# Kernel optimization log

Measured on AMD Instinct MI355X. Metric: run time of the kernel, lower is better.

Reference implementation:

```python
import jax, jax.numpy as jnp
import numpy as np

N = 50000
D = 128
E = 600000
R = 8


def setup_inputs() -> dict:
    key = jax.random.key(0)
    ks = jax.random.split(key, 8)
    x = jax.random.normal(ks[0], (N, D), dtype=jnp.float32)
    edge_index = jax.random.randint(ks[1], (2, E), 0, N, dtype=jnp.int64)
    edge_type = jax.random.randint(ks[2], (E,), 0, R, dtype=jnp.int64)
    scale = 1.0 / np.sqrt(D)
    w1 = jax.random.normal(ks[3], (R, D, D), dtype=jnp.float32) * scale
    root1 = jax.random.normal(ks[4], (D, D), dtype=jnp.float32) * scale
    b1 = jnp.zeros((D,), dtype=jnp.float32)
    w2 = jax.random.normal(ks[5], (R, D, D), dtype=jnp.float32) * scale
    root2 = jax.random.normal(ks[6], (D, D), dtype=jnp.float32) * scale
    b2 = jnp.zeros((D,), dtype=jnp.float32)
    return {"x": x, "edge_index": edge_index, "edge_type": edge_type,
            "w1": w1, "root1": root1, "b1": b1,
            "w2": w2, "root2": root2, "b2": b2}


def _rgcn_conv(x, edge_index, edge_type, w, root, b):
    # PyG RGCNConv: per-relation MEAN aggregation of source features over
    # incoming edges, then relation-specific linear, summed over relations,
    # plus root transform and bias.
    src, dst = edge_index[0], edge_index[1]
    # combined segment id: (dst_node, relation) -> one segment_sum pass
    seg = dst * R + edge_type  # [E]
    msgs = x[src]              # [E, D] gather
    sums = jax.ops.segment_sum(msgs, seg, num_segments=N * R).reshape(N, R, D)
    cnts = jax.ops.segment_sum(jnp.ones((msgs.shape[0],), dtype=x.dtype), seg,
                               num_segments=N * R).reshape(N, R, 1)
    mean = sums / jnp.maximum(cnts, 1.0)  # [N, R, D]; empty -> 0
    out = jnp.einsum('nrd,rde->ne', mean, w) + x @ root + b
    return out


def reference(x, edge_index, edge_type, w1, root1, b1, w2, root2, b2):
    # dropout is identity in eval mode
    h = jax.nn.relu(_rgcn_conv(x, edge_index, edge_type, w1, root1, b1))
    out = jax.nn.relu(_rgcn_conv(h, edge_index, edge_type, w2, root2, b2))
    return out
```

## Files before the change

### kernel.cpp

```cpp
#include <hip/hip_runtime.h>

#define NN 50000
#define D 128
#define EE 600000
#define R 8
#define NR (NN * R)
#define SCAN_CHUNK 1024
#define NSB ((NR + SCAN_CHUNK - 1) / SCAN_CHUNK)
#define KO 1152

typedef unsigned short u16;
typedef unsigned int u32;
typedef __attribute__((ext_vector_type(8))) short bf16x8;
typedef __attribute__((ext_vector_type(4))) float f32x4;

__device__ inline u16 f2bf(float f) {
    union { float f; u32 u; } v; v.f = f;
    return (u16)((v.u + 0x7FFFu + ((v.u >> 16) & 1u)) >> 16);
}
__device__ inline float bf2f(u16 h) {
    union { u32 u; float f; } v; v.u = ((u32)h) << 16;
    return v.f;
}

__global__ __launch_bounds__(256) void hist_kernel(const int* __restrict__ dst,
                                                   const int* __restrict__ et,
                                                   int* __restrict__ cnt, int E) {
    int e = blockIdx.x * 256 + threadIdx.x;
    if (e < E) atomicAdd(&cnt[dst[e] * R + et[e]], 1);
}

__global__ __launch_bounds__(256) void scanA(const int* __restrict__ cnt,
                                             int* __restrict__ off,
                                             int* __restrict__ bsum) {
    __shared__ int ts[256];
    const int b = blockIdx.x, t = threadIdx.x;
    const int base = b * SCAN_CHUNK + t * 4;
    int v0 = 0, v1 = 0, v2 = 0, v3 = 0;
    if (base + 3 < NR) {
        int4 q = *(const int4*)(cnt + base);
        v0 = q.x; v1 = q.y; v2 = q.z; v3 = q.w;
    } else {
        if (base < NR) v0 = cnt[base];
        if (base + 1 < NR) v1 = cnt[base + 1];
        if (base + 2 < NR) v2 = cnt[base + 2];
    }
    const int s = v0 + v1 + v2 + v3;
    ts[t] = s;
    __syncthreads();
    for (int d = 1; d < 256; d <<= 1) {
        int x = (t >= d) ? ts[t - d] : 0;
        __syncthreads();
        ts[t] += x;
        __syncthreads();
    }
    const int excl = ts[t] - s;
    if (base < NR) off[base] = excl;
    if (base + 1 < NR) off[base + 1] = excl + v0;
    if (base + 2 < NR) off[base + 2] = excl + v0 + v1;
    if (base + 3 < NR) off[base + 3] = excl + v0 + v1 + v2;
    if (t == 255) bsum[b] = ts[255];
}

__global__ __launch_bounds__(256) void scanBC(int* __restrict__ off,
                                              int* __restrict__ cursor,
                                              const int* __restrict__ bsum) {
    __shared__ int red[256];
    const int b = blockIdx.x, t = threadIdx.x;
    int p = 0;
    for (int i = t; i < b; i += 256) p += bsum[i];
    red[t] = p;
    __syncthreads();
    for (int d = 128; d > 0; d >>= 1) {
        if (t < d) red[t] += red[t + d];
        __syncthreads();
    }
    const int add = red[0];
    const int base = b * SCAN_CHUNK + t * 4;
#pragma unroll
    for (int j = 0; j < 4; ++j)
        if (base + j < NR) {
            int v = off[base + j] + add;
            off[base + j] = v;
            cursor[base + j] = v;
        }
    if (b == 0 && t == 0) off[NR] = EE;
}

__global__ __launch_bounds__(256) void place_kernel(const int* __restrict__ src,
                                                    const int* __restrict__ dst,
                                                    const int* __restrict__ et,
                                                    int* __restrict__ cursor,
                                                    u32* __restrict__ epk, int E) {
    int e = blockIdx.x * 256 + threadIdx.x;
    if (e < E) {
        int r = et[e];
        int key = dst[e] * R + r;
        int p = atomicAdd(&cursor[key], 1);
        epk[p] = ((u32)src[e] << 3) | (u32)r;
    }
}

__global__ __launch_bounds__(256) void bprep2_kernel(const float* __restrict__ w1,
                                                     const float* __restrict__ root1,
                                                     u16* __restrict__ Bf1,
                                                     const float* __restrict__ w2,
                                                     const float* __restrict__ root2,
                                                     u16* __restrict__ Bf2,
                                                     int4* __restrict__ cntz) {
    int gidx = blockIdx.x * 256 + threadIdx.x;
    for (int i = gidx; i < NR / 4; i += 36864)
        cntz[i] = make_int4(0, 0, 0, 0);
    if (gidx >= 2 * 9 * 4 * 8 * 64) return;
    const int layer = gidx / (9 * 4 * 8 * 64);
    const int idx = gidx - layer * (9 * 4 * 8 * 64);
    const float* w = layer ? w2 : w1;
    const float* root = layer ? root2 : root1;
    u16* Bfrag = layer ? Bf2 : Bf1;
    const int lane = idx & 63;
    const int g = (idx >> 6) & 7;
    const int kc = (idx >> 9) & 3;
    const int ct = idx >> 11;
    const int col = ct * 128 + g * 16 + (lane & 15);
    const int kbase = kc * 32 + (lane >> 4) * 8;
    u16* o = Bfrag + (size_t)idx * 8;
#pragma unroll
    for (int j = 0; j < 8; ++j) {
        const int k = kbase + j;
        float v = (col < R * D) ? w[(size_t)(col >> 7) * (D * D) + (size_t)k * D + (col & 127)]
                                : root[(size_t)k * D + (col - R * D)];
        o[j] = f2bf(v);
    }
}

template <bool INF32>
__global__ __launch_bounds__(256, 4) void gemm_xw(const void* __restrict__ xin,
                                                  const u16* __restrict__ Bfrag,
                                                  u16* __restrict__ y) {
    __shared__ uint4 Bs[2048];

    const int t = threadIdx.x;
    const int wave = t >> 6;
    const int lane = t & 63;
    const int quad = lane >> 4;
    const int l15 = lane & 15;
    const int n0 = blockIdx.x * 64;
    const int n = n0 + wave * 16 + l15;
    const int nc = (n < NN) ? n : (NN - 1);

    bf16x8 a0, a1, a2, a3;
    if (INF32) {
        const float* xr = (const float*)xin + (size_t)nc * D + quad * 8;
#pragma unroll
        for (int c = 0; c < 4; ++c) {
            float4 v0 = *(const float4*)(xr + c * 32);
            float4 v1 = *(const float4*)(xr + c * 32 + 4);
            bf16x8 a;
            a[0] = (short)f2bf(v0.x); a[1] = (short)f2bf(v0.y);
            a[2] = (short)f2bf(v0.z); a[3] = (short)f2bf(v0.w);
            a[4] = (short)f2bf(v1.x); a[5] = (short)f2bf(v1.y);
            a[6] = (short)f2bf(v1.z); a[7] = (short)f2bf(v1.w);
            if (c == 0) a0 = a; else if (c == 1) a1 = a;
            else if (c == 2) a2 = a; else a3 = a;
        }
    } else {
        const u16* xr = (const u16*)xin + (size_t)nc * D + quad * 8;
        a0 = *(const bf16x8*)(xr);
        a1 = *(const bf16x8*)(xr + 32);
        a2 = *(const bf16x8*)(xr + 64);
        a3 = *(const bf16x8*)(xr + 96);
    }

#pragma unroll 1
    for (int ct = 0; ct < 9; ++ct) {
        const uint4* bsrc = (const uint4*)Bfrag + (size_t)ct * 2048 + t;

        __syncthreads();
#pragma unroll
        for (int i = 0; i < 8; ++i) Bs[t + 256 * i] = bsrc[256 * i];
        __syncthreads();

        f32x4 acc[8];
#pragma unroll
        for (int g = 0; g < 8; ++g) acc[g] = (f32x4){0.f, 0.f, 0.f, 0.f};

        const u16* bb = (const u16*)Bs + lane * 8;
#pragma unroll
        for (int g = 0; g < 8; ++g) {
            bf16x8 b0 = *(const bf16x8*)(bb + (0 * 8 + g) * 512);
            acc[g] = __builtin_amdgcn_mfma_f32_16x16x32_bf16(a0, b0, acc[g], 0, 0, 0);
            bf16x8 b1 = *(const bf16x8*)(bb + (1 * 8 + g) * 512);
            acc[g] = __builtin_amdgcn_mfma_f32_16x16x32_bf16(a1, b1, acc[g], 0, 0, 0);
            bf16x8 b2 = *(const bf16x8*)(bb + (2 * 8 + g) * 512);
            acc[g] = __builtin_amdgcn_mfma_f32_16x16x32_bf16(a2, b2, acc[g], 0, 0, 0);
            bf16x8 b3 = *(const bf16x8*)(bb + (3 * 8 + g) * 512);
            acc[g] = __builtin_amdgcn_mfma_f32_16x16x32_bf16(a3, b3, acc[g], 0, 0, 0);
        }

#pragma unroll
        for (int g = 0; g < 8; ++g) {
            const int col = ct * 128 + g * 16 + l15;
#pragma unroll
            for (int q = 0; q < 4; ++q) {
                const int row = n0 + wave * 16 + quad * 4 + q;
                if (row < NN)
                    y[(size_t)row * KO + col] = f2bf(acc[g][q]);
            }
        }
    }
}

template <bool OUTBF>
__global__ __launch_bounds__(256) void agg_kernel(const u32* __restrict__ yv,
                                                  const int* __restrict__ off,
                                                  const u32* __restrict__ epk,
                                                  const int* __restrict__ cnt,
                                                  const float* __restrict__ bias,
                                                  void* __restrict__ outp) {
    const int n = blockIdx.x * 4 + (threadIdx.x >> 6);
    const int lane = threadIdx.x & 63;
    const int e0 = off[n * 8], e1 = off[n * 8 + 8];

    float ax = 0.f, ay = 0.f;
    int cbase = e0;
    u32 yoff = 0u; float sc = 0.f;
    if (cbase + lane < e1) {
        const u32 pk = epk[cbase + lane];
        const int r = (int)(pk & 7u);
        yoff = (pk >> 3) * (KO / 2) + (u32)r * (D / 2);
        sc = 1.0f / (float)cnt[n * 8 + r];
    }

    int i = e0;
    while (i < e1) {
        const int chunk_end = (e1 < cbase + 64) ? e1 : (cbase + 64);
        for (; i + 3 < chunk_end; i += 4) {
            const int j = i - cbase;
            const u32 p0 = (u32)__shfl((int)yoff, j);
            const u32 p1 = (u32)__shfl((int)yoff, j + 1);
            const u32 p2 = (u32)__shfl((int)yoff, j + 2);
            const u32 p3 = (u32)__shfl((int)yoff, j + 3);
            const float f0 = __shfl(sc, j);
            const float f1 = __shfl(sc, j + 1);
            const float f2 = __shfl(sc, j + 2);
            const float f3 = __shfl(sc, j + 3);
            const u32 v0 = yv[(size_t)p0 + lane];
            const u32 v1 = yv[(size_t)p1 + lane];
            const u32 v2 = yv[(size_t)p2 + lane];
            const u32 v3 = yv[(size_t)p3 + lane];
            ax += f0 * bf2f((u16)(v0 & 0xFFFFu)); ay += f0 * bf2f((u16)(v0 >> 16));
            ax += f1 * bf2f((u16)(v1 & 0xFFFFu)); ay += f1 * bf2f((u16)(v1 >> 16));
            ax += f2 * bf2f((u16)(v2 & 0xFFFFu)); ay += f2 * bf2f((u16)(v2 >> 16));
            ax += f3 * bf2f((u16)(v3 & 0xFFFFu)); ay += f3 * bf2f((u16)(v3 >> 16));
        }
        for (; i < chunk_end; ++i) {
            const int j = i - cbase;
            const u32 p0 = (u32)__shfl((int)yoff, j);
            const float f0 = __shfl(sc, j);
            const u32 v0 = yv[(size_t)p0 + lane];
            ax += f0 * bf2f((u16)(v0 & 0xFFFFu));
            ay += f0 * bf2f((u16)(v0 >> 16));
        }
        if (i < e1) {
            cbase += 64;
            if (cbase + lane < e1) {
                const u32 pk = epk[cbase + lane];
                const int r = (int)(pk & 7u);
                yoff = (pk >> 3) * (KO / 2) + (u32)r * (D / 2);
                sc = 1.0f / (float)cnt[n * 8 + r];
            } else { yoff = 0u; sc = 0.f; }
        }
    }

    const u32 rv = yv[(size_t)n * (KO / 2) + (R * D / 2) + lane];
    const float2 bb = ((const float2*)bias)[lane];
    const float ox = fmaxf(ax + bf2f((u16)(rv & 0xFFFFu)) + bb.x, 0.f);
    const float oy = fmaxf(ay + bf2f((u16)(rv >> 16)) + bb.y, 0.f);
    if (OUTBF)
        ((u32*)outp)[(size_t)n * 64 + lane] = (u32)f2bf(ox) | ((u32)f2bf(oy) << 16);
    else
        ((float2*)outp)[(size_t)n * 64 + lane] = make_float2(ox, oy);
}

extern "C" void kernel_launch(void* const* d_in, const int* in_sizes, int n_in,
                              void* d_out, int out_size, void* d_ws, size_t ws_size,
                              hipStream_t stream) {
    const float* x = (const float*)d_in[0];
    const int* ei = (const int*)d_in[1];
    const int* et = (const int*)d_in[2];
    const float* w1 = (const float*)d_in[3];
    const float* root1 = (const float*)d_in[4];
    const float* b1 = (const float*)d_in[5];
    const float* w2 = (const float*)d_in[6];
    const float* root2 = (const float*)d_in[7];
    const float* b2 = (const float*)d_in[8];
    float* out = (float*)d_out;

    char* ws = (char*)d_ws;
    int* off    = (int*)(ws + 0);
    int* cnt_i  = (int*)(ws + 1600512);
    int* cursor = (int*)(ws + 3200512);
    int* bsum   = (int*)(ws + 4800512);
    u32* epk    = (u32*)(ws + 4804096);
    u32* h      = (u32*)(ws + 7204096);
    u16* y      = (u16*)(ws + 20004096);
    u16* Bf1    = (u16*)(ws + 135204096);
    u16* Bf2    = (u16*)(ws + 135499008);

    const int* srcp = ei;
    const int* dstp = ei + EE;

    bprep2_kernel<<<144, 256, 0, stream>>>(w1, root1, Bf1, w2, root2, Bf2,
                                           (int4*)cnt_i);
    hist_kernel<<<(EE + 255) / 256, 256, 0, stream>>>(dstp, et, cnt_i, EE);
    scanA<<<NSB, 256, 0, stream>>>(cnt_i, off, bsum);
    scanBC<<<NSB, 256, 0, stream>>>(off, cursor, bsum);
    place_kernel<<<(EE + 255) / 256, 256, 0, stream>>>(srcp, dstp, et, cursor,
                                                       epk, EE);

    const int gemm_blocks = (NN + 63) / 64;
    const int agg_blocks = NN / 4;

    gemm_xw<true><<<gemm_blocks, 256, 0, stream>>>(x, Bf1, y);
    agg_kernel<true><<<agg_blocks, 256, 0, stream>>>((const u32*)y, off, epk,
                                                     cnt_i, b1, h);

    gemm_xw<false><<<gemm_blocks, 256, 0, stream>>>(h, Bf2, y);
    agg_kernel<false><<<agg_blocks, 256, 0, stream>>>((const u32*)y, off, epk,
                                                      cnt_i, b2, out);
}
```

Measured before the change: 284.2 us.

## Switch node-weight GEMM to 32x32x16 bf16 MFMA with 2x2 wave tiling

```diff
diff --git a/kernel.cpp b/kernel.cpp
--- a/kernel.cpp
+++ b/kernel.cpp
@@ -12,7 +12,7 @@
 typedef unsigned short u16;
 typedef unsigned int u32;
 typedef __attribute__((ext_vector_type(8))) short bf16x8;
-typedef __attribute__((ext_vector_type(4))) float f32x4;
+typedef __attribute__((ext_vector_type(16))) float f32x16;
 
 __device__ inline u16 f2bf(float f) {
     union { float f; u32 u; } v; v.f = f;
@@ -111,18 +111,18 @@
     int gidx = blockIdx.x * 256 + threadIdx.x;
     for (int i = gidx; i < NR / 4; i += 36864)
         cntz[i] = make_int4(0, 0, 0, 0);
-    if (gidx >= 2 * 9 * 4 * 8 * 64) return;
-    const int layer = gidx / (9 * 4 * 8 * 64);
-    const int idx = gidx - layer * (9 * 4 * 8 * 64);
+    if (gidx >= 2 * 9 * 8 * 4 * 64) return;
+    const int layer = gidx / (9 * 8 * 4 * 64);
+    const int idx = gidx - layer * (9 * 8 * 4 * 64);
     const float* w = layer ? w2 : w1;
     const float* root = layer ? root2 : root1;
     u16* Bfrag = layer ? Bf2 : Bf1;
     const int lane = idx & 63;
-    const int g = (idx >> 6) & 7;
-    const int kc = (idx >> 9) & 3;
+    const int cg = (idx >> 6) & 3;
+    const int ks = (idx >> 8) & 7;
     const int ct = idx >> 11;
-    const int col = ct * 128 + g * 16 + (lane & 15);
-    const int kbase = kc * 32 + (lane >> 4) * 8;
+    const int col = ct * 128 + cg * 32 + (lane & 31);
+    const int kbase = ks * 16 + (lane >> 5) * 8;
     u16* o = Bfrag + (size_t)idx * 8;
 #pragma unroll
     for (int j = 0; j < 8; ++j) {
@@ -134,7 +134,7 @@
 }
 
 template <bool INF32>
-__global__ __launch_bounds__(256, 4) void gemm_xw(const void* __restrict__ xin,
+__global__ __launch_bounds__(256, 3) void gemm_xw(const void* __restrict__ xin,
                                                   const u16* __restrict__ Bfrag,
                                                   u16* __restrict__ y) {
     __shared__ uint4 Bs[2048];
@@ -142,33 +142,33 @@
     const int t = threadIdx.x;
     const int wave = t >> 6;
     const int lane = t & 63;
-    const int quad = lane >> 4;
-    const int l15 = lane & 15;
+    const int l31 = lane & 31;
+    const int lh = lane >> 5;
+    const int rh = wave >> 1;
+    const int ch = wave & 1;
     const int n0 = blockIdx.x * 64;
-    const int n = n0 + wave * 16 + l15;
-    const int nc = (n < NN) ? n : (NN - 1);
-
-    bf16x8 a0, a1, a2, a3;
+    const int m = n0 + rh * 32 + l31;
+    const int mc = (m < NN) ? m : (NN - 1);
+
+    bf16x8 af[8];
     if (INF32) {
-        const float* xr = (const float*)xin + (size_t)nc * D + quad * 8;
-#pragma unroll
-        for (int c = 0; c < 4; ++c) {
-            float4 v0 = *(const float4*)(xr + c * 32);
-            float4 v1 = *(const float4*)(xr + c * 32 + 4);
+        const float* xr = (const float*)xin + (size_t)mc * D + lh * 8;
+#pragma unroll
+        for (int ks = 0; ks < 8; ++ks) {
+            float4 v0 = *(const float4*)(xr + ks * 16);
+            float4 v1 = *(const float4*)(xr + ks * 16 + 4);
             bf16x8 a;
             a[0] = (short)f2bf(v0.x); a[1] = (short)f2bf(v0.y);
             a[2] = (short)f2bf(v0.z); a[3] = (short)f2bf(v0.w);
             a[4] = (short)f2bf(v1.x); a[5] = (short)f2bf(v1.y);
             a[6] = (short)f2bf(v1.z); a[7] = (short)f2bf(v1.w);
-            if (c == 0) a0 = a; else if (c == 1) a1 = a;
-            else if (c == 2) a2 = a; else a3 = a;
+            af[ks] = a;
         }
     } else {
-        const u16* xr = (const u16*)xin + (size_t)nc * D + quad * 8;
-        a0 = *(const bf16x8*)(xr);
-        a1 = *(const bf16x8*)(xr + 32);
-        a2 = *(const bf16x8*)(xr + 64);
-        a3 = *(const bf16x8*)(xr + 96);
+        const u16* xr = (const u16*)xin + (size_t)mc * D + lh * 8;
+#pragma unroll
+        for (int ks = 0; ks < 8; ++ks)
+            af[ks] = *(const bf16x8*)(xr + ks * 16);
     }
 
 #pragma unroll 1
@@ -180,31 +180,25 @@
         for (int i = 0; i < 8; ++i) Bs[t + 256 * i] = bsrc[256 * i];
         __syncthreads();
 
-        f32x4 acc[8];
-#pragma unroll
-        for (int g = 0; g < 8; ++g) acc[g] = (f32x4){0.f, 0.f, 0.f, 0.f};
-
-        const u16* bb = (const u16*)Bs + lane * 8;
-#pragma unroll
-        for (int g = 0; g < 8; ++g) {
-            bf16x8 b0 = *(const bf16x8*)(bb + (0 * 8 + g) * 512);
-            acc[g] = __builtin_amdgcn_mfma_f32_16x16x32_bf16(a0, b0, acc[g], 0, 0, 0);
-            bf16x8 b1 = *(const bf16x8*)(bb + (1 * 8 + g) * 512);
-            acc[g] = __builtin_amdgcn_mfma_f32_16x16x32_bf16(a1, b1, acc[g], 0, 0, 0);
-            bf16x8 b2 = *(const bf16x8*)(bb + (2 * 8 + g) * 512);
-            acc[g] = __builtin_amdgcn_mfma_f32_16x16x32_bf16(a2, b2, acc[g], 0, 0, 0);
-            bf16x8 b3 = *(const bf16x8*)(bb + (3 * 8 + g) * 512);
-            acc[g] = __builtin_amdgcn_mfma_f32_16x16x32_bf16(a3, b3, acc[g], 0, 0, 0);
-        }
-
-#pragma unroll
-        for (int g = 0; g < 8; ++g) {
-            const int col = ct * 128 + g * 16 + l15;
-#pragma unroll
-            for (int q = 0; q < 4; ++q) {
-                const int row = n0 + wave * 16 + quad * 4 + q;
-                if (row < NN)
-                    y[(size_t)row * KO + col] = f2bf(acc[g][q]);
+        f32x16 acc0 = (f32x16)(0.f), acc1 = (f32x16)(0.f);
+        const u16* bb = (const u16*)Bs + (size_t)(ch * 2) * 512 + lane * 8;
+#pragma unroll
+        for (int ks = 0; ks < 8; ++ks) {
+            bf16x8 b0 = *(const bf16x8*)(bb + (size_t)ks * 2048);
+            acc0 = __builtin_amdgcn_mfma_f32_32x32x16_bf16(af[ks], b0, acc0, 0, 0, 0);
+            bf16x8 b1 = *(const bf16x8*)(bb + (size_t)ks * 2048 + 512);
+            acc1 = __builtin_amdgcn_mfma_f32_32x32x16_bf16(af[ks], b1, acc1, 0, 0, 0);
+        }
+
+        const int colb = ct * 128 + ch * 64 + l31;
+#pragma unroll
+        for (int reg = 0; reg < 16; ++reg) {
+            const int rl = (reg & 3) + 8 * (reg >> 2) + 4 * lh;
+            const int grow = n0 + rh * 32 + rl;
+            if (grow < NN) {
+                u16* yp = y + (size_t)grow * KO + colb;
+                yp[0] = f2bf(acc0[reg]);
+                yp[32] = f2bf(acc1[reg]);
             }
         }
     }
```

New measurement: 289.4 us. No clear change (+1.8%).
